# Optimization experiments

Measured on AMD Instinct MI355X. Metric: run time of the kernel, lower is better.

The kernel has to match this reference:

```python
import jax, jax.numpy as jnp
import numpy as np

S, B, D, H, L = 512, 1, 1024, 1024, 2  # seq, batch(=1 forced by view([1,-1])), input, hidden, layers


def _lstm_scan(xs, w_ih, w_hh, b, reverse=False):
    """Run an LSTMCell over xs [S,1,in]; returns (h_final, c_final, outs [S,1,H]).
    Torch LSTMCell gate order: i, f, g, o. b = b_ih + b_hh (combined)."""
    Hd = w_hh.shape[1]
    def step(carry, x):
        h, c = carry
        gates = x @ w_ih.T + h @ w_hh.T + b  # [1, 4H]
        i, f, g, o = jnp.split(gates, 4, axis=-1)
        c = jax.nn.sigmoid(f) * c + jax.nn.sigmoid(i) * jnp.tanh(g)
        h = jax.nn.sigmoid(o) * jnp.tanh(c)
        return (h, c), h
    init = (jnp.zeros((1, Hd), xs.dtype), jnp.zeros((1, Hd), xs.dtype))
    (h, c), outs = jax.lax.scan(step, init, xs, reverse=reverse)
    return h, c, outs


def setup_inputs() -> dict:
    key = jax.random.key(0)
    ks = jax.random.split(key, 13)
    sc = lambda fan_in: 1.0 / np.sqrt(fan_in)
    def W(k, rows, cols):
        return jax.random.uniform(k, (rows, cols), jnp.float32, -sc(cols), sc(cols))
    inp = {"x": jax.random.normal(ks[0], (S, B, D), jnp.float32)}
    # layer 0 (input D), fwd and bwd cells
    inp["w_ih0f"] = W(ks[1], 4 * H, D); inp["w_hh0f"] = W(ks[2], 4 * H, H)
    inp["b0f"] = jnp.zeros((4 * H,), jnp.float32)
    inp["w_ih0b"] = W(ks[3], 4 * H, D); inp["w_hh0b"] = W(ks[4], 4 * H, H)
    inp["b0b"] = jnp.zeros((4 * H,), jnp.float32)
    # layer 1 (input 2H from bidirectional concat)
    inp["w_ih1f"] = W(ks[5], 4 * H, 2 * H); inp["w_hh1f"] = W(ks[6], 4 * H, H)
    inp["b1f"] = jnp.zeros((4 * H,), jnp.float32)
    inp["w_ih1b"] = W(ks[7], 4 * H, 2 * H); inp["w_hh1b"] = W(ks[8], 4 * H, H)
    inp["b1b"] = jnp.zeros((4 * H,), jnp.float32)
    return inp


def reference(x, w_ih0f, w_hh0f, b0f, w_ih0b, w_hh0b, b0b,
              w_ih1f, w_hh1f, b1f, w_ih1b, w_hh1b, b1b):
    xs = x.reshape(x.shape[0], 1, -1)  # view([1,-1]) per step with batch=1
    # layer 0
    hf0, cf0, outs_f = _lstm_scan(xs, w_ih0f, w_hh0f, b0f, reverse=False)
    hb0, cb0, outs_b = _lstm_scan(xs, w_ih0b, w_hh0b, b0b, reverse=True)
    outs0 = jnp.concatenate([outs_f, outs_b], axis=-1)  # [S,1,2H]
    # layer 1 runs on layer-0 concat outputs; NOTE: due to a bug in the original
    # (output_sequence never reset), outputs_concat after layer 1 reuses layer-0
    # outputs, so the returned sequence is outs0, while layer-1 contributes only
    # its final hidden/cell states.
    hf1, cf1, _ = _lstm_scan(outs0, w_ih1f, w_hh1f, b1f, reverse=False)
    hb1, cb1, _ = _lstm_scan(outs0, w_ih1b, w_hh1b, b1b, reverse=True)
    final_h = jnp.stack([jnp.concatenate([hf0, hb0], axis=0),
                         jnp.concatenate([hf1, hb1], axis=0)])  # [L,2,H]
    final_c = jnp.stack([jnp.concatenate([cf0, cb0], axis=0),
                         jnp.concatenate([cf1, cb1], axis=0)])  # [L,2,H]
    return final_h, final_c, outs0
```

## Files before the change

kernel.cpp:

```cpp
#include <hip/hip_runtime.h>

#define SEQ 512
#define CAN 0x7FC0DEADu
#define NRECUR 256
#define NGEMM  256
#define CNT_FULL 16384u

#define LDA(p)   __hip_atomic_load((p), __ATOMIC_RELAXED, __HIP_MEMORY_SCOPE_AGENT)
#define STA(p,v) __hip_atomic_store((p), (v), __ATOMIC_RELAXED, __HIP_MEMORY_SCOPE_AGENT)

__device__ __forceinline__ bool has_can(unsigned long long v) {
    return ((unsigned)v == CAN) | ((unsigned)(v >> 32) == CAN);
}
__device__ __forceinline__ bool has_can4(float4 v) {
    return (__float_as_uint(v.x) == CAN) | (__float_as_uint(v.y) == CAN) |
           (__float_as_uint(v.z) == CAN) | (__float_as_uint(v.w) == CAN);
}

__global__ __launch_bounds__(256) void init_bufs(
    unsigned* __restrict__ flags, unsigned* __restrict__ hist_u,
    unsigned* __restrict__ h1_u)
{
    int i = blockIdx.x * 256 + threadIdx.x;
    if (i < 2080) flags[i] = 0u;
    int stride = gridDim.x * 256;
    for (int k = i; k < 512 * 2048; k += stride) {
        hist_u[k] = CAN;
        h1_u[k]   = CAN;
    }
}

template<bool XATOMIC>
__device__ void gemm_tile(const float* __restrict__ X, const float* __restrict__ W,
                          const float* __restrict__ bias, float* __restrict__ G,
                          int m0, int n0, int K,
                          float (*__restrict__ Xs)[68], float (*__restrict__ Ws)[68])
{
    int tid = threadIdx.x;
    int tx = tid & 15, ty = tid >> 4;
    int row = tid >> 2, kq = (tid & 3) << 2;
    float acc[4][4] = {};
    for (int k0 = 0; k0 < K; k0 += 16) {
        float4 vx;
        if (XATOMIC) {
            const float4* xp4 = (const float4*)(X + (size_t)(m0 + row) * K + k0 + kq);
            vx = *xp4;
            if (has_can4(vx)) {
                const unsigned long long* xp = (const unsigned long long*)xp4;
                unsigned long long u0, u1;
                for (;;) {
                    u0 = LDA(xp); u1 = LDA(xp + 1);
                    if (!(has_can(u0) | has_can(u1))) break;
                }
                vx.x = __uint_as_float((unsigned)u0);
                vx.y = __uint_as_float((unsigned)(u0 >> 32));
                vx.z = __uint_as_float((unsigned)u1);
                vx.w = __uint_as_float((unsigned)(u1 >> 32));
            }
        } else {
            vx = *(const float4*)(X + (size_t)(m0 + row) * K + k0 + kq);
        }
        Xs[kq + 0][row] = vx.x; Xs[kq + 1][row] = vx.y;
        Xs[kq + 2][row] = vx.z; Xs[kq + 3][row] = vx.w;
        float4 vw = *(const float4*)(W + (size_t)(n0 + row) * K + k0 + kq);
        Ws[kq + 0][row] = vw.x; Ws[kq + 1][row] = vw.y;
        Ws[kq + 2][row] = vw.z; Ws[kq + 3][row] = vw.w;
        __syncthreads();
        #pragma unroll
        for (int k = 0; k < 16; ++k) {
            float4 av = *(const float4*)&Xs[k][ty * 4];
            float4 bv = *(const float4*)&Ws[k][tx * 4];
            float a[4] = {av.x, av.y, av.z, av.w};
            float b[4] = {bv.x, bv.y, bv.z, bv.w};
            #pragma unroll
            for (int i = 0; i < 4; ++i)
                #pragma unroll
                for (int j = 0; j < 4; ++j)
                    acc[i][j] = fmaf(a[i], b[j], acc[i][j]);
        }
        __syncthreads();
    }
    #pragma unroll
    for (int i = 0; i < 4; ++i) {
        int m = m0 + ty * 4 + i;
        int n = n0 + tx * 4;
        #pragma unroll
        for (int jp = 0; jp < 2; ++jp) {
            float lo = acc[i][jp * 2]     + bias[n + jp * 2];
            float hi = acc[i][jp * 2 + 1] + bias[n + jp * 2 + 1];
            unsigned long long pk = (unsigned long long)__float_as_uint(lo) |
                                    ((unsigned long long)__float_as_uint(hi) << 32);
            STA((unsigned long long*)&G[(size_t)m * 4096 + n + jp * 2], pk);
        }
    }
}

__device__ void wait_outs0(const unsigned* __restrict__ flags0, int rc)
{
    unsigned tf = (unsigned)(64 * rc + 64);
    unsigned tb = (unsigned)(512 - 64 * rc);
    int tid = threadIdx.x;
    if (tid < 64) {
        const unsigned* ff = flags0 + tid * 4;
        const unsigned* fb = flags0 + 512 + tid * 4;
        for (;;) {
            unsigned a0 = LDA(ff), a1 = LDA(ff + 256);
            unsigned b0 = LDA(fb), b1 = LDA(fb + 256);
            if (__all(a0 >= tf && a1 >= tf && b0 >= tb && b1 >= tb)) break;
            __builtin_amdgcn_s_sleep(64);
        }
    }
    __syncthreads();
}

__device__ void recur_cell(
    const float* __restrict__ Gin, const float* __restrict__ Wh,
    float* __restrict__ hio, float* __restrict__ finh, float* __restrict__ finc,
    unsigned* __restrict__ myflags, const unsigned* __restrict__ gcnt,
    int cell, int gblk, float4* __restrict__ h4s, float* __restrict__ part)
{
    int tid = threadIdx.x;
    int j0 = gblk << 3;
    int tr = tid & 31, chunk = tid >> 5;
    int grow = ((tr >> 3) << 10) + j0 + (tr & 7);

    const float4* wrow = (const float4*)(Wh + (size_t)grow * 1024) + (chunk << 5);
    float4 w[32];
    #pragma unroll
    for (int i = 0; i < 32; ++i) w[i] = wrow[i];
    #pragma unroll
    for (int i = 0; i < 32; ++i)
        asm volatile("" : "+v"(w[i].x), "+v"(w[i].y), "+v"(w[i].z), "+v"(w[i].w));

    float cprev = 0.f;

    for (int it = 0; it < SEQ; ++it) {
        int t = cell ? (SEQ - 1 - it) : it;

        if ((it & 63) == 0 && tid < 32) {
            const unsigned* cp = gcnt + (t >> 6);
            while (LDA(cp) < CNT_FULL) __builtin_amdgcn_s_sleep(8);
        }
        float gpre = 0.f;
        if (tid < 32)
            gpre = __uint_as_float(LDA((const unsigned*)Gin + (size_t)t * 4096 + grow));

        if (it == 0) {
            h4s[tid] = make_float4(0.f, 0.f, 0.f, 0.f);
        } else {
            const float* hp = cell ? (hio + (size_t)(t + 1) * 2048 + 1024)
                                   : (hio + (size_t)(t - 1) * 2048);
            const unsigned long long* hp64 = (const unsigned long long*)hp;
            unsigned long long u0, u1;
            for (;;) {
                u0 = LDA(hp64 + 2 * tid);
                u1 = LDA(hp64 + 2 * tid + 1);
                if (!(has_can(u0) | has_can(u1))) break;
            }
            h4s[tid] = make_float4(__uint_as_float((unsigned)u0),
                                   __uint_as_float((unsigned)(u0 >> 32)),
                                   __uint_as_float((unsigned)u1),
                                   __uint_as_float((unsigned)(u1 >> 32)));
        }
        __syncthreads();

        float a0 = 0.f, a1 = 0.f, a2 = 0.f, a3 = 0.f;
        const float4* hc = h4s + (chunk << 5);
        #pragma unroll
        for (int i = 0; i < 32; i += 4) {
            float4 h0 = hc[i], h1 = hc[i + 1], h2 = hc[i + 2], h3 = hc[i + 3];
            a0 = fmaf(w[i].x, h0.x, a0);     a0 = fmaf(w[i].y, h0.y, a0);
            a0 = fmaf(w[i].z, h0.z, a0);     a0 = fmaf(w[i].w, h0.w, a0);
            a1 = fmaf(w[i+1].x, h1.x, a1);   a1 = fmaf(w[i+1].y, h1.y, a1);
            a1 = fmaf(w[i+1].z, h1.z, a1);   a1 = fmaf(w[i+1].w, h1.w, a1);
            a2 = fmaf(w[i+2].x, h2.x, a2);   a2 = fmaf(w[i+2].y, h2.y, a2);
            a2 = fmaf(w[i+2].z, h2.z, a2);   a2 = fmaf(w[i+2].w, h2.w, a2);
            a3 = fmaf(w[i+3].x, h3.x, a3);   a3 = fmaf(w[i+3].y, h3.y, a3);
            a3 = fmaf(w[i+3].z, h3.z, a3);   a3 = fmaf(w[i+3].w, h3.w, a3);
        }
        part[chunk * 33 + tr] = (a0 + a1) + (a2 + a3);
        __syncthreads();

        if (tid < 32) {
            float v = gpre;
            #pragma unroll
            for (int k = 0; k < 8; ++k) v += part[k * 33 + tid];
            bool isg = (tid >> 3) == 2;
            float s = isg ? 2.f : 1.f;
            float e = __expf(-s * v);
            float r = 1.f / (1.f + e);
            float a = isg ? 2.f * r - 1.f : r;
            float si = __shfl(a, (tid & 7) + 0);
            float sf = __shfl(a, (tid & 7) + 8);
            float tg = __shfl(a, (tid & 7) + 16);
            float so = __shfl(a, (tid & 7) + 24);
            if (tid < 8) {
                float cnew = sf * cprev + si * tg;
                float e2 = __expf(-2.f * cnew);
                float hnew = so * (2.f / (1.f + e2) - 1.f);
                cprev = cnew;
                int j = j0 + tid;
                STA(&hio[(size_t)t * 2048 + cell * 1024 + j], hnew);
                if (it == SEQ - 1) {
                    STA(&finh[j], hnew);
                    STA(&finc[j], cnew);
                }
            }
            if (tid == 0)
                STA(&myflags[gblk * 4], (unsigned)(it + 1));
        }
    }
}

__constant__ int korder[8] = {3, 4, 2, 5, 1, 6, 0, 7};

__global__ __launch_bounds__(256, 2) void lstm_fused(
    const float* __restrict__ x,
    const float* __restrict__ w_ih0f, const float* __restrict__ w_hh0f, const float* __restrict__ b0f,
    const float* __restrict__ w_ih0b, const float* __restrict__ w_hh0b, const float* __restrict__ b0b,
    const float* __restrict__ w_ih1f, const float* __restrict__ w_hh1f, const float* __restrict__ b1f,
    const float* __restrict__ w_ih1b, const float* __restrict__ w_hh1b, const float* __restrict__ b1b,
    float* __restrict__ G0f, float* __restrict__ G0b,
    float* __restrict__ hist, float* __restrict__ h1buf,
    float* __restrict__ out,
    unsigned* __restrict__ flags0, unsigned* __restrict__ flags1,
    unsigned* __restrict__ g0cnt, unsigned* __restrict__ g1cnt)
{
    __shared__ float4 h4s[256];
    __shared__ float part[8 * 33];
    __shared__ float Xs[16][68];
    __shared__ float Ws[16][68];

    int bid = blockIdx.x;
    if (bid < NRECUR) {
        __builtin_amdgcn_s_setprio(1);
        int cell = (bid >> 7) & 1;
        int gblk = bid & 127;
        recur_cell(cell ? G0b : G0f, cell ? w_hh0b : w_hh0f, hist,
                   out + cell * 1024, out + 4096 + cell * 1024,
                   flags0 + cell * 512, g0cnt + cell * 8, cell, gblk, h4s, part);
        recur_cell(cell ? G0b : G0f, cell ? w_hh1b : w_hh1f, h1buf,
                   out + 2048 + cell * 1024, out + 4096 + 2048 + cell * 1024,
                   flags1 + cell * 512, g1cnt + cell * 8, cell, gblk, h4s, part);
    } else {
        int gid = bid - NRECUR;
        for (int idx = gid; idx < 1024; idx += NGEMM) {
            int k = idx >> 7, half = (idx >> 6) & 1, cc = idx & 63;
            int rc = half ? (7 - k) : k;
            gemm_tile<false>(x, half ? w_ih0b : w_ih0f, half ? b0b : b0f,
                             half ? G0b : G0f, rc * 64, cc * 64, 1024, Xs, Ws);
            __hip_atomic_fetch_add(&g0cnt[half * 8 + rc], 1u,
                                   __ATOMIC_RELEASE, __HIP_MEMORY_SCOPE_AGENT);
        }
        for (int idx = gid; idx < 1024; idx += NGEMM) {
            int k = korder[idx >> 7], half = (idx >> 6) & 1, cc = idx & 63;
            int rc = half ? (7 - k) : k;
            wait_outs0(flags0, rc);
            gemm_tile<true>(hist, half ? w_ih1b : w_ih1f, half ? b1b : b1f,
                            half ? G0b : G0f, rc * 64, cc * 64, 2048, Xs, Ws);
            __hip_atomic_fetch_add(&g1cnt[half * 8 + rc], 1u,
                                   __ATOMIC_RELEASE, __HIP_MEMORY_SCOPE_AGENT);
        }
    }
}

__global__ __launch_bounds__(256) void gemm_bias2(
    const float* __restrict__ X,
    const float* __restrict__ Wf, const float* __restrict__ Wb,
    const float* __restrict__ biasf, const float* __restrict__ biasb,
    float* __restrict__ Gf, float* __restrict__ Gb,
    int M, int N, int K)
{
    const float* W    = blockIdx.z ? Wb : Wf;
    const float* bias = blockIdx.z ? biasb : biasf;
    float*       G    = blockIdx.z ? Gb : Gf;
    __shared__ float Xs[16][68];
    __shared__ float Ws[16][68];
    int tid = threadIdx.x;
    int tx = tid & 15, ty = tid >> 4;
    int m0 = blockIdx.y * 64, n0 = blockIdx.x * 64;
    float acc[4][4] = {};
    for (int k0 = 0; k0 < K; k0 += 16) {
        int row = tid >> 2, kq = (tid & 3) << 2;
        float4 vx = *(const float4*)(X + (size_t)(m0 + row) * K + k0 + kq);
        Xs[kq + 0][row] = vx.x; Xs[kq + 1][row] = vx.y;
        Xs[kq + 2][row] = vx.z; Xs[kq + 3][row] = vx.w;
        float4 vw = *(const float4*)(W + (size_t)(n0 + row) * K + k0 + kq);
        Ws[kq + 0][row] = vw.x; Ws[kq + 1][row] = vw.y;
        Ws[kq + 2][row] = vw.z; Ws[kq + 3][row] = vw.w;
        __syncthreads();
        #pragma unroll
        for (int k = 0; k < 16; ++k) {
            float4 av = *(const float4*)&Xs[k][ty * 4];
            float4 bv = *(const float4*)&Ws[k][tx * 4];
            float a[4] = {av.x, av.y, av.z, av.w};
            float b[4] = {bv.x, bv.y, bv.z, bv.w};
            #pragma unroll
            for (int i = 0; i < 4; ++i)
                #pragma unroll
                for (int j = 0; j < 4; ++j)
                    acc[i][j] = fmaf(a[i], b[j], acc[i][j]);
        }
        __syncthreads();
    }
    #pragma unroll
    for (int i = 0; i < 4; ++i) {
        int m = m0 + ty * 4 + i;
        #pragma unroll
        for (int j = 0; j < 4; ++j) {
            int n = n0 + tx * 4 + j;
            G[(size_t)m * N + n] = acc[i][j] + bias[n];
        }
    }
}

__global__ __launch_bounds__(256, 1) void lstm_recur(
    const float* __restrict__ Gf, const float* __restrict__ Gb,
    const float* __restrict__ Whf, const float* __restrict__ Whb,
    float* __restrict__ hist, float* __restrict__ h1buf,
    float* __restrict__ fin_h, float* __restrict__ fin_c,
    unsigned* __restrict__ flags, int layer)
{
    __shared__ float4 h4s[256];
    __shared__ float part[8 * 33];
    __shared__ float c_s[8];

    int tid = threadIdx.x;
    int cell = blockIdx.x >> 7;
    int gblk = blockIdx.x & 127;
    int j0 = gblk << 3;

    const float* Wh  = cell ? Whb : Whf;
    const float* Gin = cell ? Gb  : Gf;
    unsigned* myflags = flags + cell * 512;
    float* hout = (layer == 0) ? hist : h1buf;

    int tr = tid & 31, chunk = tid >> 5;
    int grow = ((tr >> 3) << 10) + j0 + (tr & 7);

    const float4* wrow = (const float4*)(Wh + (size_t)grow * 1024) + (chunk << 5);
    float4 w[32];
    #pragma unroll
    for (int i = 0; i < 32; ++i) w[i] = wrow[i];
    #pragma unroll
    for (int i = 0; i < 32; ++i)
        asm volatile("" : "+v"(w[i].x), "+v"(w[i].y), "+v"(w[i].z), "+v"(w[i].w));

    if (tid < 8) c_s[tid] = 0.f;

    for (int it = 0; it < SEQ; ++it) {
        int t = cell ? (SEQ - 1 - it) : it;
        float gpre = 0.f;
        if (tid < 32) gpre = Gin[(size_t)t * 4096 + grow];

        if (it == 0) {
            h4s[tid] = make_float4(0.f, 0.f, 0.f, 0.f);
        } else {
            if (tid < 64) {
                const unsigned* f0 = myflags + tid * 4;
                const unsigned* f1 = myflags + 256 + tid * 4;
                unsigned tgt = (unsigned)it;
                for (;;) {
                    unsigned a = LDA(f0);
                    unsigned b = LDA(f1);
                    if (__all(a >= tgt && b >= tgt)) break;
                    __builtin_amdgcn_s_sleep(1);
                }
            }
            __syncthreads();
            const float* hp;
            if (layer == 0)
                hp = cell ? (hist + (size_t)(t + 1) * 2048 + 1024)
                          : (hist + (size_t)(t - 1) * 2048);
            else
                hp = cell ? (h1buf + (size_t)(t + 1) * 2048 + 1024)
                          : (h1buf + (size_t)(t - 1) * 2048);
            const unsigned long long* hp64 = (const unsigned long long*)hp;
            unsigned long long u0, u1;
            for (;;) {
                u0 = LDA(hp64 + 2 * tid);
                u1 = LDA(hp64 + 2 * tid + 1);
                if (!(has_can(u0) | has_can(u1))) break;
            }
            h4s[tid] = make_float4(__uint_as_float((unsigned)u0),
                                   __uint_as_float((unsigned)(u0 >> 32)),
                                   __uint_as_float((unsigned)u1),
                                   __uint_as_float((unsigned)(u1 >> 32)));
        }
        __syncthreads();

        float a0 = 0.f, a1 = 0.f, a2 = 0.f, a3 = 0.f;
        const float4* hc = (const float4*)h4s + (chunk << 5);
        #pragma unroll
        for (int i = 0; i < 32; i += 4) {
            float4 h0 = hc[i], h1 = hc[i + 1], h2 = hc[i + 2], h3 = hc[i + 3];
            a0 = fmaf(w[i].x, h0.x, a0);     a0 = fmaf(w[i].y, h0.y, a0);
            a0 = fmaf(w[i].z, h0.z, a0);     a0 = fmaf(w[i].w, h0.w, a0);
            a1 = fmaf(w[i+1].x, h1.x, a1);   a1 = fmaf(w[i+1].y, h1.y, a1);
            a1 = fmaf(w[i+1].z, h1.z, a1);   a1 = fmaf(w[i+1].w, h1.w, a1);
            a2 = fmaf(w[i+2].x, h2.x, a2);   a2 = fmaf(w[i+2].y, h2.y, a2);
            a2 = fmaf(w[i+2].z, h2.z, a2);   a2 = fmaf(w[i+2].w, h2.w, a2);
            a3 = fmaf(w[i+3].x, h3.x, a3);   a3 = fmaf(w[i+3].y, h3.y, a3);
            a3 = fmaf(w[i+3].z, h3.z, a3);   a3 = fmaf(w[i+3].w, h3.w, a3);
        }
        part[chunk * 33 + tr] = (a0 + a1) + (a2 + a3);
        __syncthreads();

        if (tid < 32) {
            float v = gpre;
            #pragma unroll
            for (int k = 0; k < 8; ++k) v += part[k * 33 + tid];
            bool isg = (tid >> 3) == 2;
            float s = isg ? 2.f : 1.f;
            float e = __expf(-s * v);
            float r = 1.f / (1.f + e);
            float a = isg ? 2.f * r - 1.f : r;
            float si = __shfl(a, (tid & 7) + 0);
            float sf = __shfl(a, (tid & 7) + 8);
            float tg = __shfl(a, (tid & 7) + 16);
            float so = __shfl(a, (tid & 7) + 24);
            if (tid < 8) {
                float cnew = sf * c_s[tid] + si * tg;
                float e2 = __expf(-2.f * cnew);
                float hnew = so * (2.f / (1.f + e2) - 1.f);
                c_s[tid] = cnew;
                int j = j0 + tid;
                STA(&hout[(size_t)t * 2048 + cell * 1024 + j], hnew);
                if (it == SEQ - 1) {
                    STA(&fin_h[cell * 1024 + j], hnew);
                    STA(&fin_c[cell * 1024 + j], cnew);
                }
            }
            if (tid == 0 && it < SEQ - 1)
                STA(&myflags[gblk * 4], (unsigned)(it + 1));
        }
    }
}

extern "C" void kernel_launch(void* const* d_in, const int* in_sizes, int n_in,
                              void* d_out, int out_size, void* d_ws, size_t ws_size,
                              hipStream_t stream) {
    const float* x      = (const float*)d_in[0];
    const float* w_ih0f = (const float*)d_in[1];
    const float* w_hh0f = (const float*)d_in[2];
    const float* b0f    = (const float*)d_in[3];
    const float* w_ih0b = (const float*)d_in[4];
    const float* w_hh0b = (const float*)d_in[5];
    const float* b0b    = (const float*)d_in[6];
    const float* w_ih1f = (const float*)d_in[7];
    const float* w_hh1f = (const float*)d_in[8];
    const float* b1f    = (const float*)d_in[9];
    const float* w_ih1b = (const float*)d_in[10];
    const float* w_hh1b = (const float*)d_in[11];
    const float* b1b    = (const float*)d_in[12];

    float* out   = (float*)d_out;
    float* outs0 = out + 8192;
    float* ws    = (float*)d_ws;
    float* G0f   = ws;
    float* G0b   = ws + (size_t)512 * 4096;
    float* h1buf = ws + (size_t)2 * 512 * 4096;
    unsigned* flagbase = (unsigned*)(h1buf + (size_t)512 * 2048);
    unsigned* flags0 = flagbase;
    unsigned* flags1 = flagbase + 1024;
    unsigned* g0cnt  = flagbase + 2048;
    unsigned* g1cnt  = flagbase + 2064;

    hipLaunchKernelGGL(init_bufs, dim3(1024), dim3(256), 0, stream,
                       flagbase, (unsigned*)outs0, (unsigned*)h1buf);

    int occ = 0;
    hipOccupancyMaxActiveBlocksPerMultiprocessor(&occ, lstm_fused, 256, 0);

    hipError_t lerr = hipErrorUnknown;
    if (occ >= 2) {
        const float* xp = x;
        const float* a1 = w_ih0f; const float* a2 = w_hh0f; const float* a3 = b0f;
        const float* a4 = w_ih0b; const float* a5 = w_hh0b; const float* a6 = b0b;
        const float* a7 = w_ih1f; const float* a8 = w_hh1f; const float* a9 = b1f;
        const float* aa = w_ih1b; const float* ab = w_hh1b; const float* ac = b1b;
        float* g0fp = G0f; float* g0bp = G0b;
        float* histp = outs0; float* h1p = h1buf; float* outp = out;
        unsigned* f0p = flags0; unsigned* f1p = flags1;
        unsigned* c0p = g0cnt;  unsigned* c1p = g1cnt;
        void* args[] = {(void*)&xp,
                        (void*)&a1, (void*)&a2, (void*)&a3,
                        (void*)&a4, (void*)&a5, (void*)&a6,
                        (void*)&a7, (void*)&a8, (void*)&a9,
                        (void*)&aa, (void*)&ab, (void*)&ac,
                        (void*)&g0fp, (void*)&g0bp,
                        (void*)&histp, (void*)&h1p, (void*)&outp,
                        (void*)&f0p, (void*)&f1p, (void*)&c0p, (void*)&c1p};
        lerr = hipLaunchCooperativeKernel((void*)lstm_fused, dim3(NRECUR + NGEMM),
                                          dim3(256), args, 0, stream);
    }
    if (occ < 2 || lerr != hipSuccess) {
        float* G1f = ws;
        float* G1b = ws + (size_t)512 * 4096;
        dim3 gb(64, 8, 2), tb(256);
        hipLaunchKernelGGL(gemm_bias2, gb, tb, 0, stream,
                           x, w_ih0f, w_ih0b, b0f, b0b, G0f, G0b, 512, 4096, 1024);
        {
            int layer = 0;
            const float* Gfp = G0f; const float* Gbp = G0b;
            const float* Whf = w_hh0f; const float* Whb = w_hh0b;
            float* hist = outs0; float* h1 = h1buf;
            float* finh = out;
            float* finc = out + 4096;
            unsigned* fl = flags0;
            void* args[] = {(void*)&Gfp, (void*)&Gbp, (void*)&Whf, (void*)&Whb,
                            (void*)&hist, (void*)&h1, (void*)&finh, (void*)&finc,
                            (void*)&fl, (void*)&layer};
            hipLaunchCooperativeKernel((void*)lstm_recur, dim3(256), dim3(256), args, 0, stream);
        }
        hipLaunchKernelGGL(gemm_bias2, gb, tb, 0, stream,
                           outs0, w_ih1f, w_ih1b, b1f, b1b, G1f, G1b, 512, 4096, 2048);
        {
            int layer = 1;
            const float* Gfp = G1f; const float* Gbp = G1b;
            const float* Whf = w_hh1f; const float* Whb = w_hh1b;
            float* hist = outs0; float* h1 = h1buf;
            float* finh = out + 2048;
            float* finc = out + 4096 + 2048;
            unsigned* fl = flags1;
            void* args[] = {(void*)&Gfp, (void*)&Gbp, (void*)&Whf, (void*)&Whb,
                            (void*)&hist, (void*)&h1, (void*)&finh, (void*)&finc,
                            (void*)&fl, (void*)&layer};
            hipLaunchCooperativeKernel((void*)lstm_recur, dim3(256), dim3(256), args, 0, stream);
        }
    }
}
```

Baseline: 2.506 ms.

## Reduce LSTM recurrent dot products with wave shuffles instead of shared-memory partials

Remaps threads so the 8 threads sharing a gate row sit in adjacent lanes of one wave, and sums their partial dot products with xor shuffles. This removes the shared-memory partial buffer and the extra barrier before a single 32-thread gate stage; each half-wave now handles one hidden unit's gates and cell update. The shared h buffer is padded to 33 float4 per chunk to avoid bank conflicts, and a barrier is added before it is overwritten so the previous step's readers are done. This trades one serialized reduction phase for more shuffles and more threads running the activation math.

Result: no change. 2.532 ms (+1.0%).

```diff
diff --git a/kernel.cpp b/kernel.cpp
--- a/kernel.cpp
+++ b/kernel.cpp
@@ -117,14 +117,15 @@
     const float* __restrict__ Gin, const float* __restrict__ Wh,
     float* __restrict__ hio, float* __restrict__ finh, float* __restrict__ finc,
     unsigned* __restrict__ myflags, const unsigned* __restrict__ gcnt,
-    int cell, int gblk, float4* __restrict__ h4s, float* __restrict__ part)
+    int cell, int gblk, float4 (*__restrict__ h4s)[33])
 {
     int tid = threadIdx.x;
     int j0 = gblk << 3;
-    int tr = tid & 31, chunk = tid >> 5;
-    int grow = ((tr >> 3) << 10) + j0 + (tr & 7);
-
-    const float4* wrow = (const float4*)(Wh + (size_t)grow * 1024) + (chunk << 5);
+    int r = tid >> 3;
+    int c = tid & 7;
+    int grow = ((r & 3) << 10) + j0 + (r >> 2);
+
+    const float4* wrow = (const float4*)(Wh + (size_t)grow * 1024) + (c << 5);
     float4 w[32];
     #pragma unroll
     for (int i = 0; i < 32; ++i) w[i] = wrow[i];
@@ -133,20 +134,23 @@
         asm volatile("" : "+v"(w[i].x), "+v"(w[i].y), "+v"(w[i].z), "+v"(w[i].w));
 
     float cprev = 0.f;
+    int lane = tid & 63;
+    int u = tid >> 5;
 
     for (int it = 0; it < SEQ; ++it) {
         int t = cell ? (SEQ - 1 - it) : it;
 
-        if ((it & 63) == 0 && tid < 32) {
+        if ((it & 63) == 0 && c == 0) {
             const unsigned* cp = gcnt + (t >> 6);
             while (LDA(cp) < CNT_FULL) __builtin_amdgcn_s_sleep(8);
         }
         float gpre = 0.f;
-        if (tid < 32)
+        if (c == 0)
             gpre = __uint_as_float(LDA((const unsigned*)Gin + (size_t)t * 4096 + grow));
 
+        float4 hreg;
         if (it == 0) {
-            h4s[tid] = make_float4(0.f, 0.f, 0.f, 0.f);
+            hreg = make_float4(0.f, 0.f, 0.f, 0.f);
         } else {
             const float* hp = cell ? (hio + (size_t)(t + 1) * 2048 + 1024)
                                    : (hio + (size_t)(t - 1) * 2048);
@@ -157,58 +161,59 @@
                 u1 = LDA(hp64 + 2 * tid + 1);
                 if (!(has_can(u0) | has_can(u1))) break;
             }
-            h4s[tid] = make_float4(__uint_as_float((unsigned)u0),
-                                   __uint_as_float((unsigned)(u0 >> 32)),
-                                   __uint_as_float((unsigned)u1),
-                                   __uint_as_float((unsigned)(u1 >> 32)));
-        }
+            hreg = make_float4(__uint_as_float((unsigned)u0),
+                               __uint_as_float((unsigned)(u0 >> 32)),
+                               __uint_as_float((unsigned)u1),
+                               __uint_as_float((unsigned)(u1 >> 32)));
+        }
+        __syncthreads();
+        h4s[tid >> 5][tid & 31] = hreg;
         __syncthreads();
 
         float a0 = 0.f, a1 = 0.f, a2 = 0.f, a3 = 0.f;
-        const float4* hc = h4s + (chunk << 5);
+        const float4* hc = h4s[c];
         #pragma unroll
-        for (int i = 0; i < 32; i += 4) {
-            float4 h0 = hc[i], h1 = hc[i + 1], h2 = hc[i + 2], h3 = hc[i + 3];
-            a0 = fmaf(w[i].x, h0.x, a0);     a0 = fmaf(w[i].y, h0.y, a0);
-            a0 = fmaf(w[i].z, h0.z, a0);     a0 = fmaf(w[i].w, h0.w, a0);
-            a1 = fmaf(w[i+1].x, h1.x, a1);   a1 = fmaf(w[i+1].y, h1.y, a1);
-            a1 = fmaf(w[i+1].z, h1.z, a1);   a1 = fmaf(w[i+1].w, h1.w, a1);
-            a2 = fmaf(w[i+2].x, h2.x, a2);   a2 = fmaf(w[i+2].y, h2.y, a2);
-            a2 = fmaf(w[i+2].z, h2.z, a2);   a2 = fmaf(w[i+2].w, h2.w, a2);
-            a3 = fmaf(w[i+3].x, h3.x, a3);   a3 = fmaf(w[i+3].y, h3.y, a3);
-            a3 = fmaf(w[i+3].z, h3.z, a3);   a3 = fmaf(w[i+3].w, h3.w, a3);
-        }
-        part[chunk * 33 + tr] = (a0 + a1) + (a2 + a3);
-        __syncthreads();
-
-        if (tid < 32) {
-            float v = gpre;
-            #pragma unroll
-            for (int k = 0; k < 8; ++k) v += part[k * 33 + tid];
-            bool isg = (tid >> 3) == 2;
-            float s = isg ? 2.f : 1.f;
-            float e = __expf(-s * v);
-            float r = 1.f / (1.f + e);
-            float a = isg ? 2.f * r - 1.f : r;
-            float si = __shfl(a, (tid & 7) + 0);
-            float sf = __shfl(a, (tid & 7) + 8);
-            float tg = __shfl(a, (tid & 7) + 16);
-            float so = __shfl(a, (tid & 7) + 24);
-            if (tid < 8) {
-                float cnew = sf * cprev + si * tg;
-                float e2 = __expf(-2.f * cnew);
-                float hnew = so * (2.f / (1.f + e2) - 1.f);
-                cprev = cnew;
-                int j = j0 + tid;
-                STA(&hio[(size_t)t * 2048 + cell * 1024 + j], hnew);
-                if (it == SEQ - 1) {
-                    STA(&finh[j], hnew);
-                    STA(&finc[j], cnew);
-                }
+        for (int i = 0; i < 8; ++i) {
+            float4 h0 = hc[i],      h1 = hc[i + 8],
+                   h2 = hc[i + 16], h3 = hc[i + 24];
+            a0 = fmaf(w[i].x,    h0.x, a0);  a0 = fmaf(w[i].y,    h0.y, a0);
+            a0 = fmaf(w[i].z,    h0.z, a0);  a0 = fmaf(w[i].w,    h0.w, a0);
+            a1 = fmaf(w[i+8].x,  h1.x, a1);  a1 = fmaf(w[i+8].y,  h1.y, a1);
+            a1 = fmaf(w[i+8].z,  h1.z, a1);  a1 = fmaf(w[i+8].w,  h1.w, a1);
+            a2 = fmaf(w[i+16].x, h2.x, a2);  a2 = fmaf(w[i+16].y, h2.y, a2);
+            a2 = fmaf(w[i+16].z, h2.z, a2);  a2 = fmaf(w[i+16].w, h2.w, a2);
+            a3 = fmaf(w[i+24].x, h3.x, a3);  a3 = fmaf(w[i+24].y, h3.y, a3);
+            a3 = fmaf(w[i+24].z, h3.z, a3);  a3 = fmaf(w[i+24].w, h3.w, a3);
+        }
+        float v = (a0 + a1) + (a2 + a3);
+        if (c == 0) v += gpre;
+        v += __shfl_xor(v, 1);
+        v += __shfl_xor(v, 2);
+        v += __shfl_xor(v, 4);
+        bool isg = (r & 3) == 2;
+        float s = isg ? 2.f : 1.f;
+        float e = __expf(-s * v);
+        float rr = 1.f / (1.f + e);
+        float a = isg ? 2.f * rr - 1.f : rr;
+        int base = lane & 32;
+        float si = __shfl(a, base + 0);
+        float sf = __shfl(a, base + 8);
+        float tg = __shfl(a, base + 16);
+        float so = __shfl(a, base + 24);
+        if ((lane & 31) == 0) {
+            float cnew = sf * cprev + si * tg;
+            float e2 = __expf(-2.f * cnew);
+            float hnew = so * (2.f / (1.f + e2) - 1.f);
+            cprev = cnew;
+            int j = j0 + u;
+            STA(&hio[(size_t)t * 2048 + cell * 1024 + j], hnew);
+            if (it == SEQ - 1) {
+                STA(&finh[j], hnew);
+                STA(&finc[j], cnew);
             }
-            if (tid == 0)
-                STA(&myflags[gblk * 4], (unsigned)(it + 1));
-        }
+        }
+        if (tid == 0)
+            STA(&myflags[gblk * 4], (unsigned)(it + 1));
     }
 }
 
@@ -226,8 +231,7 @@
     unsigned* __restrict__ flags0, unsigned* __restrict__ flags1,
     unsigned* __restrict__ g0cnt, unsigned* __restrict__ g1cnt)
 {
-    __shared__ float4 h4s[256];
-    __shared__ float part[8 * 33];
+    __shared__ float4 h4s[8][33];
     __shared__ float Xs[16][68];
     __shared__ float Ws[16][68];
 
@@ -238,10 +242,10 @@
         int gblk = bid & 127;
         recur_cell(cell ? G0b : G0f, cell ? w_hh0b : w_hh0f, hist,
                    out + cell * 1024, out + 4096 + cell * 1024,
-                   flags0 + cell * 512, g0cnt + cell * 8, cell, gblk, h4s, part);
+                   flags0 + cell * 512, g0cnt + cell * 8, cell, gblk, h4s);
         recur_cell(cell ? G0b : G0f, cell ? w_hh1b : w_hh1f, h1buf,
                    out + 2048 + cell * 1024, out + 4096 + 2048 + cell * 1024,
-                   flags1 + cell * 512, g1cnt + cell * 8, cell, gblk, h4s, part);
+                   flags1 + cell * 512, g1cnt + cell * 8, cell, gblk, h4s);
     } else {
         int gid = bid - NRECUR;
         for (int idx = gid; idx < 1024; idx += NGEMM) {
```
